# Kernel tuning notes

Hardware: AMD Instinct MI355X
Metric: run time of the kernel (lower is better)

The kernel has to match this reference:

```python
import jax, jax.numpy as jnp
import numpy as np

W = 50          # Sakoe-Chiba window half-width (|i-j| <= W)
BIG = 1e9       # finite 'infinity' so gradients stay NaN-free
EPS = 1e-8      # matches torch.cosine_similarity eps


def setup_inputs() -> dict:
    key = jax.random.key(0)
    k1, k2 = jax.random.split(key)
    x1 = jax.random.normal(k1, (64, 512, 256), dtype=jnp.float32)
    x2 = jax.random.normal(k2, (64, 512, 256), dtype=jnp.float32)
    return {"x1": x1, "x2": x2}


def _cosine_cost(x1, x2):
    # cost[b,i,j] = 1 - cos_sim(x1[b,i], x2[b,j])
    num = jnp.einsum('bid,bjd->bij', x1, x2)
    n1 = jnp.maximum(jnp.sqrt(jnp.sum(x1 * x1, axis=-1)), EPS)  # [B,T1]
    n2 = jnp.maximum(jnp.sqrt(jnp.sum(x2 * x2, axis=-1)), EPS)  # [B,T2]
    return 1.0 - num / (n1[:, :, None] * n2[:, None, :])


def _dtw_acc(cost, w):
    # Anti-diagonal wavefront DP: acc[i,j] = cost[i,j] + min(acc[i-1,j], acc[i,j-1], acc[i-1,j-1])
    # with the Sakoe-Chiba band |i-j| <= w. Returns acc[T1-1, T2-1] per batch.
    B, T1, T2 = cost.shape
    ii = jnp.arange(T1)
    dt = cost.dtype

    def step(carry, d):
        prev1, prev2 = carry                       # diagonals d-1 and d-2, each [B,T1] indexed by i
        jj = d - ii                                # column index for each row i on diagonal d
        valid = (jj >= 0) & (jj < T2) & (jnp.abs(ii - jj) <= w)
        # gather cost[b, i, d-i]
        cdiag = jnp.take_along_axis(
            cost, jnp.clip(jj, 0, T2 - 1)[None, :, None], axis=2)[..., 0]  # [B,T1]
        pad = jnp.full((B, 1), BIG, dt)
        p1_im1 = jnp.concatenate([pad, prev1[:, :-1]], axis=1)  # acc[i-1, j]   (diag d-1, i-1)
        p2_im1 = jnp.concatenate([pad, prev2[:, :-1]], axis=1)  # acc[i-1, j-1] (diag d-2, i-1)
        m = jnp.minimum(jnp.minimum(prev1, p1_im1), p2_im1)     # prev1 = acc[i, j-1]
        m = jnp.where((ii == 0) & (jj == 0), jnp.zeros((), dt), m)  # DP origin
        new = jnp.where(valid, cdiag + m, jnp.full((), BIG, dt))
        return (new, prev1), None

    init = (jnp.full((B, T1), BIG, dt), jnp.full((B, T1), BIG, dt))
    (last, _), _ = jax.lax.scan(step, init, jnp.arange(T1 + T2 - 1))
    return last[:, T1 - 1]  # acc[-1, -1]


def reference(x1, x2):
    cost = _cosine_cost(x1, x2)       # [B,T1,T2]
    scores = _dtw_acc(cost, W)        # [B]
    return scores[:, None]            # [B,1], matches unsqueeze(-1)
```

## Files before the change

kernel.cpp:

```cpp
#include <hip/hip_runtime.h>

#define BIGF 1e9f
#define TT 512
#define DD 256
#define NB 64
#define DROWS 1088
#define SAK 40
#define CST 66

typedef float floatx16 __attribute__((ext_vector_type(16)));
typedef __bf16 bf16x8 __attribute__((ext_vector_type(8)));

__device__ __forceinline__ float dpp_wave_shr1(float x, float oldv) {
  int r = __builtin_amdgcn_update_dpp(__builtin_bit_cast(int, oldv),
                                      __builtin_bit_cast(int, x),
                                      0x138, 0xF, 0xF, false);
  return __builtin_bit_cast(float, r);
}
__device__ __forceinline__ float dpp_wave_shl1(float x, float oldv) {
  int r = __builtin_amdgcn_update_dpp(__builtin_bit_cast(int, oldv),
                                      __builtin_bit_cast(int, x),
                                      0x130, 0xF, 0xF, false);
  return __builtin_bit_cast(float, r);
}

__global__ __launch_bounds__(256) void cost_kernel(const float* __restrict__ x1,
                                                   const float* __restrict__ x2,
                                                   float* __restrict__ diag) {
  const int p = blockIdx.x;
  const int x = p & 7;
  const int pl = p >> 3;

  __shared__ __align__(16) float sC[64 * CST];
  __bf16* sA = (__bf16*)sC;
  __bf16* sB = ((__bf16*)sC) + 64 * SAK;
  __shared__ float rA[64];
  __shared__ float rB[64];

  const int t = threadIdx.x;
  const int lane = t & 63;
  const int w = t >> 6;
  const int wi = w >> 1;
  const int wj = w & 1;
  const int ln = lane & 31;
  const int kh = lane >> 5;

  const int sr = t >> 2;
  const int sq = t & 3;
  __bf16* dA = sA + sr * SAK + sq * 8;
  __bf16* dB = sB + sr * SAK + sq * 8;
  const __bf16* fAp = sA + (wi * 32 + ln) * SAK + kh * 8;
  const __bf16* fBp = sB + (wj * 32 + ln) * SAK + kh * 8;

  for (int kt = 0; kt < 2; ++kt) {
    const int T = pl + 96 * kt;
    const int bhi = T / 24;
    const int m = T - bhi * 24;
    const int b = bhi * 8 + x;
    const int it = m & 7;
    const int jt = m >> 3;
    const int i0 = it * 64;
    const int j0 = i0 - 50 + jt * 64;

    float* db = diag + (size_t)b * (DROWS * 64);

    if (m == 0) {
      for (int r = w; r < 180; r += 4) {
        const int d = (r < 64) ? r : r + 908;
        const int pp = d & 1;
        const int i = (d >> 1) + lane + pp - 25;
        const int j = d - i;
        const int k = 2 * lane + pp;
        if (k > 100 || (unsigned)i >= TT || (unsigned)j >= TT)
          db[(size_t)d * 64 + lane] = BIGF;
      }
    }

    const float* x1b = x1 + (size_t)b * (TT * DD);
    const float* x2b = x2 + (size_t)b * (TT * DD);
    int gj = j0 + sr;
    gj = gj < 0 ? 0 : (gj > TT - 1 ? TT - 1 : gj);
    const float* pAg = x1b + (size_t)(i0 + sr) * DD + sq * 8;
    const float* pBg = x2b + (size_t)gj * DD + sq * 8;

    floatx16 acc = {};
    float pa = 0.f, pb = 0.f;

    for (int kc = 0; kc < DD; kc += 32) {
      const float4 a0 = *(const float4*)(pAg + kc);
      const float4 a1 = *(const float4*)(pAg + kc + 4);
      const float4 b0 = *(const float4*)(pBg + kc);
      const float4 b1 = *(const float4*)(pBg + kc + 4);
      pa += a0.x * a0.x + a0.y * a0.y + a0.z * a0.z + a0.w * a0.w;
      pa += a1.x * a1.x + a1.y * a1.y + a1.z * a1.z + a1.w * a1.w;
      pb += b0.x * b0.x + b0.y * b0.y + b0.z * b0.z + b0.w * b0.w;
      pb += b1.x * b1.x + b1.y * b1.y + b1.z * b1.z + b1.w * b1.w;
      __syncthreads();
      {
        bf16x8 va, vb;
        va[0] = (__bf16)a0.x; va[1] = (__bf16)a0.y; va[2] = (__bf16)a0.z; va[3] = (__bf16)a0.w;
        va[4] = (__bf16)a1.x; va[5] = (__bf16)a1.y; va[6] = (__bf16)a1.z; va[7] = (__bf16)a1.w;
        vb[0] = (__bf16)b0.x; vb[1] = (__bf16)b0.y; vb[2] = (__bf16)b0.z; vb[3] = (__bf16)b0.w;
        vb[4] = (__bf16)b1.x; vb[5] = (__bf16)b1.y; vb[6] = (__bf16)b1.z; vb[7] = (__bf16)b1.w;
        *(bf16x8*)dA = va;
        *(bf16x8*)dB = vb;
      }
      __syncthreads();
      const bf16x8 fa0 = *(const bf16x8*)fAp;
      const bf16x8 fb0 = *(const bf16x8*)fBp;
      const bf16x8 fa1 = *(const bf16x8*)(fAp + 16);
      const bf16x8 fb1 = *(const bf16x8*)(fBp + 16);
      acc = __builtin_amdgcn_mfma_f32_32x32x16_bf16(fa0, fb0, acc, 0, 0, 0);
      acc = __builtin_amdgcn_mfma_f32_32x32x16_bf16(fa1, fb1, acc, 0, 0, 0);
    }

    pa += __shfl_xor(pa, 1, 64); pa += __shfl_xor(pa, 2, 64);
    pb += __shfl_xor(pb, 1, 64); pb += __shfl_xor(pb, 2, 64);
    if (sq == 0) {
      rA[sr] = 1.0f / fmaxf(sqrtf(pa), 1e-8f);
      rB[sr] = 1.0f / fmaxf(sqrtf(pb), 1e-8f);
    }
    __syncthreads();

    {
      const int rj = wj * 32 + ln;
      const float r2 = rB[rj];
#pragma unroll
      for (int reg = 0; reg < 16; ++reg) {
        const int ri = wi * 32 + (reg & 3) + 8 * (reg >> 2) + 4 * kh;
        sC[ri * CST + rj] = 1.0f - acc[reg] * rA[ri] * r2;
      }
    }
    __syncthreads();

    {
      const int d0 = i0 + j0;
      const int a65 = 65 * lane;
#pragma unroll 4
      for (int rr = 0; rr < 32; ++rr) {
        const int r = 4 * rr + w;
        const int d = d0 + r;
        const int pp = d & 1;
        const int roff = ((d + pp - 50) >> 1) - i0;
        const int ri = lane + roff;
        const int rj = r - ri;
        const int kband = 2 * lane + pp;
        const int jg = j0 + rj;
        if (((unsigned)ri < 64u) & ((unsigned)rj < 64u) & (kband <= 100) &
            ((unsigned)jg < (unsigned)TT)) {
          db[(size_t)d * 64 + lane] = sC[a65 + 65 * roff + r];
        }
      }
    }
  }
}

__global__ __launch_bounds__(64) void dtw_dp_kernel(const float* __restrict__ diag,
                                                    float* __restrict__ out) {
  const int b = blockIdx.x;
  const int l = threadIdx.x;
  const bool inv_odd = (l >= 50);
  const bool inv_even = (l >= 51);
  const float* base = diag + (size_t)b * (DROWS * 64);
  const float* pO = base + 64 + l;
  const float* pE = base + 128 + l;
  float cr[64];
#pragma unroll
  for (int t = 0; t < 32; ++t) {
    cr[2 * t] = *pO; pO += 128;
    cr[2 * t + 1] = *pE; pE += 128;
  }
  float prev2 = BIGF;
  const float c00 = base[25];
  float prev1 = (l == 25) ? c00 : BIGF;
  float ans = BIGF;
  for (int itr = 0; itr < 16; ++itr) {
#pragma unroll
    for (int u = 0; u < 32; ++u) {
      const float c1 = inv_odd ? BIGF : cr[2 * u];
      cr[2 * u] = *pO; pO += 128;
      const float sh = dpp_wave_shl1(prev1, BIGF);
      const float m3 = fminf(fminf(prev1, sh), prev2);
      prev2 = prev1;
      prev1 = c1 + m3;
      const float c2 = inv_even ? BIGF : cr[2 * u + 1];
      cr[2 * u + 1] = *pE; pE += 128;
      const float sh2 = dpp_wave_shr1(prev1, BIGF);
      const float m32 = fminf(fminf(sh2, prev1), prev2);
      prev2 = prev1;
      prev1 = c2 + m32;
      if (itr == 15 && u == 30) ans = prev1;
    }
  }
  if (l == 25) out[b] = ans;
}

extern "C" void kernel_launch(void* const* d_in, const int* in_sizes, int n_in,
                              void* d_out, int out_size, void* d_ws, size_t ws_size,
                              hipStream_t stream) {
  const float* x1 = (const float*)d_in[0];
  const float* x2 = (const float*)d_in[1];
  float* out = (float*)d_out;
  float* diag = (float*)d_ws;

  cost_kernel<<<768, 256, 0, stream>>>(x1, x2, diag);
  dtw_dp_kernel<<<NB, 64, 0, stream>>>(diag, out);
}
```

Before: 126.6 us.

## Stage DTW diagonals through double-buffered LDS with producer warps

The DP kernel becomes a 256-thread block. Three producer wavefronts prefetch 64-diagonal chunks of the cost band from global memory into a double-buffered shared-memory tile with float4 loads, while one wavefront runs the serial wavefront recurrence reading from LDS. This replaces the 64-entry register prefetch ring of per-lane scalar global loads. It aims to take global load latency off the serial DP critical path. In exchange it adds a block-wide barrier per chunk and LDS read latency on each step.

```diff
diff --git a/kernel.cpp b/kernel.cpp
--- a/kernel.cpp
+++ b/kernel.cpp
@@ -7,6 +7,7 @@
 #define DROWS 1088
 #define SAK 40
 #define CST 66
+#define CH 64
 
 typedef float floatx16 __attribute__((ext_vector_type(16)));
 typedef __bf16 bf16x8 __attribute__((ext_vector_type(8)));
@@ -155,44 +156,82 @@
   }
 }
 
-__global__ __launch_bounds__(64) void dtw_dp_kernel(const float* __restrict__ diag,
-                                                    float* __restrict__ out) {
+__global__ __launch_bounds__(256) void dtw_dp_kernel(const float* __restrict__ diag,
+                                                     float* __restrict__ out) {
+  __shared__ __align__(16) float sD[2][CH][64];
   const int b = blockIdx.x;
-  const int l = threadIdx.x;
+  const int t = threadIdx.x;
+  const float* base = diag + (size_t)b * (DROWS * 64);
+
+  const int tf = t - 64;
+
+  if (t >= 64) {
+    const float* src = base + 64;
+    float4 v[6];
+#pragma unroll
+    for (int k = 0; k < 6; ++k) {
+      const int item = tf + 192 * k;
+      if (item < 1024)
+        v[k] = *(const float4*)(src + (size_t)(item >> 4) * 64 + (item & 15) * 4);
+    }
+#pragma unroll
+    for (int k = 0; k < 6; ++k) {
+      const int item = tf + 192 * k;
+      if (item < 1024)
+        *(float4*)&sD[0][item >> 4][(item & 15) * 4] = v[k];
+    }
+  }
+
+  const int l = t;
   const bool inv_odd = (l >= 50);
   const bool inv_even = (l >= 51);
-  const float* base = diag + (size_t)b * (DROWS * 64);
-  const float* pO = base + 64 + l;
-  const float* pE = base + 128 + l;
-  float cr[64];
-#pragma unroll
-  for (int t = 0; t < 32; ++t) {
-    cr[2 * t] = *pO; pO += 128;
-    cr[2 * t + 1] = *pE; pE += 128;
+  float prev2 = BIGF;
+  float prev1 = BIGF;
+  if (t < 64) prev1 = (l == 25) ? base[25] : BIGF;
+  float ans = BIGF;
+
+  __syncthreads();
+
+  for (int c = 0; c < 16; ++c) {
+    if (t >= 64) {
+      if (c < 15) {
+        const float* src = base + (size_t)(64 * (c + 1) + 1) * 64;
+        float4 v[6];
+#pragma unroll
+        for (int k = 0; k < 6; ++k) {
+          const int item = tf + 192 * k;
+          if (item < 1024)
+            v[k] = *(const float4*)(src + (size_t)(item >> 4) * 64 + (item & 15) * 4);
+        }
+        float* dst = &sD[(c + 1) & 1][0][0];
+#pragma unroll
+        for (int k = 0; k < 6; ++k) {
+          const int item = tf + 192 * k;
+          if (item < 1024)
+            *(float4*)(dst + (size_t)(item >> 4) * 64 + (item & 15) * 4) = v[k];
+        }
+      }
+    } else {
+      const float* row = &sD[c & 1][0][0] + l;
+#pragma unroll
+      for (int s = 0; s < 64; s += 2) {
+        const float c1 = inv_odd ? BIGF : row[s * 64];
+        const float sh = dpp_wave_shl1(prev1, BIGF);
+        const float m3 = fminf(fminf(prev1, sh), prev2);
+        prev2 = prev1;
+        prev1 = c1 + m3;
+        const float c2 = inv_even ? BIGF : row[(s + 1) * 64];
+        const float sh2 = dpp_wave_shr1(prev1, BIGF);
+        const float m32 = fminf(fminf(sh2, prev1), prev2);
+        prev2 = prev1;
+        prev1 = c2 + m32;
+        if (c == 15 && s == 60) ans = prev1;
+      }
+    }
+    __syncthreads();
   }
-  float prev2 = BIGF;
-  const float c00 = base[25];
-  float prev1 = (l == 25) ? c00 : BIGF;
-  float ans = BIGF;
-  for (int itr = 0; itr < 16; ++itr) {
-#pragma unroll
-    for (int u = 0; u < 32; ++u) {
-      const float c1 = inv_odd ? BIGF : cr[2 * u];
-      cr[2 * u] = *pO; pO += 128;
-      const float sh = dpp_wave_shl1(prev1, BIGF);
-      const float m3 = fminf(fminf(prev1, sh), prev2);
-      prev2 = prev1;
-      prev1 = c1 + m3;
-      const float c2 = inv_even ? BIGF : cr[2 * u + 1];
-      cr[2 * u + 1] = *pE; pE += 128;
-      const float sh2 = dpp_wave_shr1(prev1, BIGF);
-      const float m32 = fminf(fminf(sh2, prev1), prev2);
-      prev2 = prev1;
-      prev1 = c2 + m32;
-      if (itr == 15 && u == 30) ans = prev1;
-    }
-  }
-  if (l == 25) out[b] = ans;
+
+  if (t == 25) out[b] = ans;
 }
 
 extern "C" void kernel_launch(void* const* d_in, const int* in_sizes, int n_in,
@@ -204,5 +243,5 @@
   float* diag = (float*)d_ws;
 
   cost_kernel<<<768, 256, 0, stream>>>(x1, x2, diag);
-  dtw_dp_kernel<<<NB, 64, 0, stream>>>(diag, out);
-}
+  dtw_dp_kernel<<<NB, 256, 0, stream>>>(diag, out);
+}
```

Result: slower. 153.8 us (+21.5%).
